# Performance work log

Measured on AMD Instinct MI355X. Metric: run time of the kernel, lower is better.

The kernel has to match this reference:

```python
import jax, jax.numpy as jnp
import numpy as np

N_CODES = 512
D = 8
BETA = 0.25


def setup_inputs() -> dict:
    key = jax.random.key(0)
    k1, k2 = jax.random.split(key)
    z = jax.random.normal(k1, (8, D, 16, 64, 64), dtype=jnp.float32)
    # torch init: uniform(-1/n_codes, 1/n_codes)
    codebook = jax.random.uniform(
        k2, (N_CODES, D), dtype=jnp.float32,
        minval=-1.0 / N_CODES, maxval=1.0 / N_CODES)
    return {"z": z, "codebook": codebook}


def reference(z, codebook):
    B, Dc, T, H, W = z.shape
    # [B, T, H, W, D] -> [N, D]
    z_flat = jnp.transpose(z, (0, 2, 3, 4, 1)).reshape(-1, Dc)
    z2 = jnp.sum(z_flat * z_flat, axis=1, keepdims=True)          # [N, 1]
    e2 = jnp.sum(codebook * codebook, axis=1)[None, :]            # [1, K]
    ze = z_flat @ codebook.T                                      # [N, K]
    dists = z2 + e2 - 2.0 * ze
    idx = jnp.argmin(dists, axis=1)                               # [N]
    z_q = jnp.transpose(codebook[idx].reshape(B, T, H, W, Dc), (0, 4, 1, 2, 3))
    commit = jnp.mean((jax.lax.stop_gradient(z_q) - z) ** 2)
    codebk = jnp.mean((z_q - jax.lax.stop_gradient(z)) ** 2)
    vq_loss = codebk + BETA * commit
    z_q_st = z + jax.lax.stop_gradient(z_q - z)
    return z_q_st, vq_loss, idx.reshape(B, T, H, W)
```

## Files before the change

### kernel.cpp

```cpp
#include <hip/hip_runtime.h>


#define NPTS      524288
#define KCODES    512
#define DDIM      8
#define CH_STRIDE 65536
#define B_STRIDE  524288
#define BLK       256
#define NTILES    32
#define CMAX      8
#define FLT_BIG   3.402823466e+38f

typedef short bf8 __attribute__((ext_vector_type(8)));
typedef float f4  __attribute__((ext_vector_type(4)));

__device__ __forceinline__ unsigned short f2bf(float f) {
    unsigned u = __float_as_uint(f);
    unsigned r = u + 0x7fffu + ((u >> 16) & 1u);
    return (unsigned short)(r >> 16);
}
__device__ __forceinline__ float bf2f(unsigned short h) {
    return __uint_as_float(((unsigned)h) << 16);
}

__device__ __forceinline__ float np_sumsq8(const float* x) {
    float p0 = __fmul_rn(x[0], x[0]);
    float p1 = __fmul_rn(x[1], x[1]);
    float p2 = __fmul_rn(x[2], x[2]);
    float p3 = __fmul_rn(x[3], x[3]);
    float p4 = __fmul_rn(x[4], x[4]);
    float p5 = __fmul_rn(x[5], x[5]);
    float p6 = __fmul_rn(x[6], x[6]);
    float p7 = __fmul_rn(x[7], x[7]);
    return __fadd_rn(__fadd_rn(__fadd_rn(p0, p1), __fadd_rn(p2, p3)),
                     __fadd_rn(__fadd_rn(p4, p5), __fadd_rn(p6, p7)));
}

__device__ __forceinline__ float np_dist(const float* __restrict__ cb,
                                         const float* __restrict__ e2f,
                                         int k, const float* zv, float z2) {
    const float* c = cb + (size_t)k * DDIM;
    float ze = 0.0f;
    #pragma unroll
    for (int j = 0; j < DDIM; ++j) ze = __fmaf_rn(zv[j], c[j], ze);
    return __fmaf_rn(-2.0f, ze, __fadd_rn(z2, e2f[k]));
}

__global__ void prep(const float* __restrict__ cb, float* __restrict__ e2f,
                     unsigned short* __restrict__ wsB, float* __restrict__ out_loss) {
    const int tid = blockIdx.x * 256 + threadIdx.x;
    if (tid == 0) *out_loss = 0.0f;
    const int t    = tid >> 6;
    const int lane = tid & 63;
    const int quad = lane >> 4;
    const int colc = lane & 15;
    const int n    = t * 16 + colc;
    float row[DDIM];
    #pragma unroll
    for (int j = 0; j < DDIM; ++j) row[j] = cb[n * DDIM + j];
    const float e2 = np_sumsq8(row);
    if (quad == 3) e2f[n] = e2;

    unsigned short sh[8];
    #pragma unroll
    for (int j = 0; j < 8; ++j) {
        const unsigned short eh = f2bf(row[j]);
        const unsigned short el = f2bf(__fsub_rn(row[j], bf2f(eh)));
        sh[j] = (quad == 1) ? el : eh;
    }
    if (quad == 3) {
        const unsigned short e2h = f2bf(e2);
        const unsigned short e2l = f2bf(__fsub_rn(e2, bf2f(e2h)));
        sh[0] = e2h; sh[1] = e2l;
        #pragma unroll
        for (int j = 2; j < 8; ++j) sh[j] = 0;
    }
    unsigned short* dst = wsB + (size_t)(t * 64 + lane) * 8;
    #pragma unroll
    for (int j = 0; j < 8; ++j) dst[j] = sh[j];
}

__global__ __launch_bounds__(BLK, 3) void vq_main(
    const float* __restrict__ z, const float* __restrict__ cb,
    const float* __restrict__ e2f, const unsigned short* __restrict__ wsB,
    float* __restrict__ out_zq, float* __restrict__ out_loss,
    float* __restrict__ out_idx)
{
    __shared__ unsigned short ldsB[NTILES * 64 * 8];
    __shared__ int   ccnt[BLK];
    __shared__ int   clist[BLK][CMAX];
    __shared__ float wsum[4];

    const int tid  = threadIdx.x;
    const int wave = tid >> 6;
    const int lane = tid & 63;
    const int quad = lane >> 4;
    const int col  = lane & 15;

    {
        const uint4* src = (const uint4*)wsB;
        uint4* dst = (uint4*)ldsB;
        #pragma unroll
        for (int q = 0; q < 8; ++q)
            dst[tid + q * BLK] = src[tid + q * BLK];
    }
    ccnt[tid] = 0;

    const int n = blockIdx.x * BLK + tid;
    const int b = n >> 16;
    const int s = n & 65535;
    const float* zp = z + (size_t)b * B_STRIDE + s;
    float zv[DDIM];
    #pragma unroll
    for (int j = 0; j < DDIM; ++j) zv[j] = zp[(size_t)j * CH_STRIDE];
    const float z2 = np_sumsq8(zv);

    float zmax = z2;
    #pragma unroll
    for (int mk = 1; mk <= 32; mk <<= 1) zmax = fmaxf(zmax, __shfl_xor(zmax, mk, 64));
    const float eps = zmax * 6e-7f + 3e-6f;

    bf8 af0, af1, af2, af3;
#define MK_AFRAG(AF, Q)                                                        \
    {                                                                          \
        const int srcl = (Q)*16 + col;                                         \
        _Pragma("unroll")                                                      \
        for (int j = 0; j < 8; ++j) {                                          \
            const float raw = __shfl(zv[j], srcl, 64);                         \
            const unsigned short h = f2bf(raw);                                \
            const float zh = bf2f(h);                                          \
            const float v = (quad == 2) ? __fsub_rn(raw, zh) : zh;             \
            AF[j] = (short)f2bf(-2.0f * v);                                    \
        }                                                                      \
        if (quad == 3) AF = (bf8){(short)0x3F80, (short)0x3F80, 0, 0, 0, 0, 0, 0}; \
    }
    MK_AFRAG(af0, 0) MK_AFRAG(af1, 1) MK_AFRAG(af2, 2) MK_AFRAG(af3, 3)

    __syncthreads();

    const bf8* Bp = (const bf8*)ldsB;

    f4 mn0 = (f4){FLT_BIG, FLT_BIG, FLT_BIG, FLT_BIG};
    f4 mn1 = mn0, mn2 = mn0, mn3 = mn0;
    #pragma unroll 4
    for (int t = 0; t < NTILES; ++t) {
        const bf8 bfrag = Bp[t * 64 + lane];
        f4 zero = (f4){0.0f, 0.0f, 0.0f, 0.0f};
        const f4 a0 = __builtin_amdgcn_mfma_f32_16x16x32_bf16(af0, bfrag, zero, 0, 0, 0);
        const f4 a1 = __builtin_amdgcn_mfma_f32_16x16x32_bf16(af1, bfrag, zero, 0, 0, 0);
        const f4 a2 = __builtin_amdgcn_mfma_f32_16x16x32_bf16(af2, bfrag, zero, 0, 0, 0);
        const f4 a3 = __builtin_amdgcn_mfma_f32_16x16x32_bf16(af3, bfrag, zero, 0, 0, 0);
        #pragma unroll
        for (int r = 0; r < 4; ++r) {
            mn0[r] = fminf(mn0[r], a0[r]); mn1[r] = fminf(mn1[r], a1[r]);
            mn2[r] = fminf(mn2[r], a2[r]); mn3[r] = fminf(mn3[r], a3[r]);
        }
    }
    #pragma unroll
    for (int mk = 1; mk <= 8; mk <<= 1) {
        #pragma unroll
        for (int r = 0; r < 4; ++r) {
            mn0[r] = fminf(mn0[r], __shfl_xor(mn0[r], mk, 64));
            mn1[r] = fminf(mn1[r], __shfl_xor(mn1[r], mk, 64));
            mn2[r] = fminf(mn2[r], __shfl_xor(mn2[r], mk, 64));
            mn3[r] = fminf(mn3[r], __shfl_xor(mn3[r], mk, 64));
        }
    }
    #pragma unroll
    for (int r = 0; r < 4; ++r) {
        mn0[r] += eps; mn1[r] += eps; mn2[r] += eps; mn3[r] += eps;
    }

    #pragma unroll 2
    for (int t = 0; t < NTILES; ++t) {
        const bf8 bfrag = Bp[t * 64 + lane];
        f4 zero = (f4){0.0f, 0.0f, 0.0f, 0.0f};
        const f4 a0 = __builtin_amdgcn_mfma_f32_16x16x32_bf16(af0, bfrag, zero, 0, 0, 0);
        const f4 a1 = __builtin_amdgcn_mfma_f32_16x16x32_bf16(af1, bfrag, zero, 0, 0, 0);
        const f4 a2 = __builtin_amdgcn_mfma_f32_16x16x32_bf16(af2, bfrag, zero, 0, 0, 0);
        const f4 a3 = __builtin_amdgcn_mfma_f32_16x16x32_bf16(af3, bfrag, zero, 0, 0, 0);
        const int code = t * 16 + col;
        const int pb   = wave * 64 + quad * 4;
#define PUSH(AQ, MQ, Q)                                                        \
    {                                                                          \
        const bool c0 = AQ[0] <= MQ[0], c1 = AQ[1] <= MQ[1];                   \
        const bool c2 = AQ[2] <= MQ[2], c3 = AQ[3] <= MQ[3];                   \
        if (c0 | c1 | c2 | c3) {                                               \
            const int pt = pb + (Q)*16;                                        \
            if (c0) { int p = atomicAdd(&ccnt[pt + 0], 1); if (p < CMAX) clist[pt + 0][p] = code; } \
            if (c1) { int p = atomicAdd(&ccnt[pt + 1], 1); if (p < CMAX) clist[pt + 1][p] = code; } \
            if (c2) { int p = atomicAdd(&ccnt[pt + 2], 1); if (p < CMAX) clist[pt + 2][p] = code; } \
            if (c3) { int p = atomicAdd(&ccnt[pt + 3], 1); if (p < CMAX) clist[pt + 3][p] = code; } \
        }                                                                      \
    }
        PUSH(a0, mn0, 0) PUSH(a1, mn1, 1) PUSH(a2, mn2, 2) PUSH(a3, mn3, 3)
    }
    __syncthreads();

    const int cnt = ccnt[tid];
    float best = FLT_BIG;
    int   bidx = 0;
    if (cnt <= CMAX) {
        for (int i = 0; i < cnt; ++i) {
            const int k = clist[tid][i];
            const float d = np_dist(cb, e2f, k, zv, z2);
            if (d < best || (d == best && k < bidx)) { best = d; bidx = k; }
        }
    } else {
        for (int k = 0; k < KCODES; ++k) {
            const float d = np_dist(cb, e2f, k, zv, z2);
            if (d < best) { best = d; bidx = k; }
        }
    }
    out_idx[n] = (float)bidx;

    const float* cw = cb + (size_t)bidx * DDIM;
    float* op = out_zq + (size_t)b * B_STRIDE + s;
    float lsum = 0.0f;
    #pragma unroll
    for (int j = 0; j < DDIM; ++j) {
        const float zq = cw[j];
        const float t  = __fsub_rn(zq, zv[j]);
        op[(size_t)j * CH_STRIDE] = __fadd_rn(zv[j], t);
        lsum = __fmaf_rn(t, t, lsum);
    }

    #pragma unroll
    for (int off = 32; off > 0; off >>= 1) lsum += __shfl_down(lsum, off, 64);
    if (lane == 0) wsum[wave] = lsum;
    __syncthreads();
    if (tid == 0) {
        const float bs = (wsum[0] + wsum[1]) + (wsum[2] + wsum[3]);
        atomicAdd(out_loss, bs * (1.25f / 4194304.0f));
    }
}

extern "C" void kernel_launch(void* const* d_in, const int* in_sizes, int n_in,
                              void* d_out, int out_size, void* d_ws, size_t ws_size,
                              hipStream_t stream) {
    const float* z  = (const float*)d_in[0];
    const float* cb = (const float*)d_in[1];
    float* out      = (float*)d_out;
    float* out_zq   = out;
    float* out_loss = out + 4194304;
    float* out_idx  = out + 4194305;
    float* e2f            = (float*)d_ws;
    unsigned short* wsB   = (unsigned short*)((char*)d_ws + 2048);

    prep<<<8, 256, 0, stream>>>(cb, e2f, wsB, out_loss);
    vq_main<<<NPTS / BLK, BLK, 0, stream>>>(z, cb, e2f, wsB,
                                            out_zq, out_loss, out_idx);
}
```

Before: 136.8 us.

## Replace LDS atomics with ballot-based candidate scan and shrink candidate lists

The candidate collection now uses a wave ballot per row, and one lane per row walks the set bits to append code indices, replacing per-element LDS atomicAdd. The candidate list shrinks to 4 unsigned shorts per point. Launch bounds rise to 4 blocks per CU, and the A-fragment hi/lo bf16 split is precomputed once and shuffled as packed words. A single-candidate fast path skips the exact distance recheck. The risks are that points with more than 4 candidates fall back to the full 512-code scan, and that skipping the recheck relies on the eps filter being exact.

```diff
diff --git a/kernel.cpp b/kernel.cpp
--- a/kernel.cpp
+++ b/kernel.cpp
@@ -8,7 +8,7 @@
 #define B_STRIDE  524288
 #define BLK       256
 #define NTILES    32
-#define CMAX      8
+#define CMAX      4
 #define FLT_BIG   3.402823466e+38f
 
 typedef short bf8 __attribute__((ext_vector_type(8)));
@@ -80,16 +80,16 @@
     for (int j = 0; j < 8; ++j) dst[j] = sh[j];
 }
 
-__global__ __launch_bounds__(BLK, 3) void vq_main(
+__global__ __launch_bounds__(BLK, 4) void vq_main(
     const float* __restrict__ z, const float* __restrict__ cb,
     const float* __restrict__ e2f, const unsigned short* __restrict__ wsB,
     float* __restrict__ out_zq, float* __restrict__ out_loss,
     float* __restrict__ out_idx)
 {
     __shared__ unsigned short ldsB[NTILES * 64 * 8];
-    __shared__ int   ccnt[BLK];
-    __shared__ int   clist[BLK][CMAX];
-    __shared__ float wsum[4];
+    __shared__ int            ccnt[BLK];
+    __shared__ unsigned short clist[BLK][CMAX];
+    __shared__ float          wsum[4];
 
     const int tid  = threadIdx.x;
     const int wave = tid >> 6;
@@ -119,6 +119,17 @@
     #pragma unroll
     for (int mk = 1; mk <= 32; mk <<= 1) zmax = fmaxf(zmax, __shfl_xor(zmax, mk, 64));
     const float eps = zmax * 6e-7f + 3e-6f;
+
+    unsigned pkz[8];
+    #pragma unroll
+    for (int j = 0; j < 8; ++j) {
+        const unsigned short hh = f2bf(zv[j]);
+        const float zh = bf2f(hh);
+        const float zl = __fsub_rn(zv[j], zh);
+        const unsigned short ah = f2bf(-2.0f * zh);
+        const unsigned short al = f2bf(-2.0f * zl);
+        pkz[j] = (unsigned)ah | ((unsigned)al << 16);
+    }
 
     bf8 af0, af1, af2, af3;
 #define MK_AFRAG(AF, Q)                                                        \
@@ -126,11 +137,9 @@
         const int srcl = (Q)*16 + col;                                         \
         _Pragma("unroll")                                                      \
         for (int j = 0; j < 8; ++j) {                                          \
-            const float raw = __shfl(zv[j], srcl, 64);                         \
-            const unsigned short h = f2bf(raw);                                \
-            const float zh = bf2f(h);                                          \
-            const float v = (quad == 2) ? __fsub_rn(raw, zh) : zh;             \
-            AF[j] = (short)f2bf(-2.0f * v);                                    \
+            const unsigned w = (unsigned)__shfl((int)pkz[j], srcl, 64);        \
+            const unsigned us = (quad == 2) ? (w >> 16) : (w & 0xFFFFu);       \
+            AF[j] = (short)us;                                                 \
         }                                                                      \
         if (quad == 3) AF = (bf8){(short)0x3F80, (short)0x3F80, 0, 0, 0, 0, 0, 0}; \
     }
@@ -171,6 +180,7 @@
         mn0[r] += eps; mn1[r] += eps; mn2[r] += eps; mn3[r] += eps;
     }
 
+    const int pbase = wave * 64 + quad * 4;
     #pragma unroll 2
     for (int t = 0; t < NTILES; ++t) {
         const bf8 bfrag = Bp[t * 64 + lane];
@@ -179,34 +189,43 @@
         const f4 a1 = __builtin_amdgcn_mfma_f32_16x16x32_bf16(af1, bfrag, zero, 0, 0, 0);
         const f4 a2 = __builtin_amdgcn_mfma_f32_16x16x32_bf16(af2, bfrag, zero, 0, 0, 0);
         const f4 a3 = __builtin_amdgcn_mfma_f32_16x16x32_bf16(af3, bfrag, zero, 0, 0, 0);
-        const int code = t * 16 + col;
-        const int pb   = wave * 64 + quad * 4;
-#define PUSH(AQ, MQ, Q)                                                        \
+#define SCAN(AQ, MQ, Q)                                                        \
     {                                                                          \
-        const bool c0 = AQ[0] <= MQ[0], c1 = AQ[1] <= MQ[1];                   \
-        const bool c2 = AQ[2] <= MQ[2], c3 = AQ[3] <= MQ[3];                   \
-        if (c0 | c1 | c2 | c3) {                                               \
-            const int pt = pb + (Q)*16;                                        \
-            if (c0) { int p = atomicAdd(&ccnt[pt + 0], 1); if (p < CMAX) clist[pt + 0][p] = code; } \
-            if (c1) { int p = atomicAdd(&ccnt[pt + 1], 1); if (p < CMAX) clist[pt + 1][p] = code; } \
-            if (c2) { int p = atomicAdd(&ccnt[pt + 2], 1); if (p < CMAX) clist[pt + 2][p] = code; } \
-            if (c3) { int p = atomicAdd(&ccnt[pt + 3], 1); if (p < CMAX) clist[pt + 3][p] = code; } \
+        _Pragma("unroll")                                                      \
+        for (int r = 0; r < 4; ++r) {                                          \
+            const unsigned long long m = __ballot(AQ[r] <= MQ[r]);             \
+            if (col == 0) {                                                    \
+                unsigned sl = (unsigned)(m >> (quad * 16)) & 0xFFFFu;          \
+                if (sl) {                                                      \
+                    const int pt = pbase + (Q)*16 + r;                         \
+                    int c = ccnt[pt];                                          \
+                    do {                                                       \
+                        const int bcol = __builtin_ctz(sl); sl &= sl - 1;      \
+                        if (c < CMAX) clist[pt][c] = (unsigned short)(t * 16 + bcol); \
+                        ++c;                                                   \
+                    } while (sl);                                              \
+                    ccnt[pt] = c;                                              \
+                }                                                              \
+            }                                                                  \
         }                                                                      \
     }
-        PUSH(a0, mn0, 0) PUSH(a1, mn1, 1) PUSH(a2, mn2, 2) PUSH(a3, mn3, 3)
+        SCAN(a0, mn0, 0) SCAN(a1, mn1, 1) SCAN(a2, mn2, 2) SCAN(a3, mn3, 3)
     }
     __syncthreads();
 
     const int cnt = ccnt[tid];
-    float best = FLT_BIG;
-    int   bidx = 0;
-    if (cnt <= CMAX) {
+    int bidx;
+    if (cnt == 1) {
+        bidx = clist[tid][0];
+    } else if (cnt <= CMAX) {
+        float best = FLT_BIG; bidx = 0;
         for (int i = 0; i < cnt; ++i) {
             const int k = clist[tid][i];
             const float d = np_dist(cb, e2f, k, zv, z2);
             if (d < best || (d == best && k < bidx)) { best = d; bidx = k; }
         }
     } else {
+        float best = FLT_BIG; bidx = 0;
         for (int k = 0; k < KCODES; ++k) {
             const float d = np_dist(cb, e2f, k, zv, z2);
             if (d < best) { best = d; bidx = k; }
```

New measurement: 164.5 us. 1.2x slower.
